# Optimization experiments

Measured on AMD Instinct MI355X. Metric: run time of the kernel, lower is better.

## Reference

```python
import jax, jax.numpy as jnp
import numpy as np

N, E, C, R = 10000, 160000, 128, 8
D = 4 * C  # 128x0e + 128x1o -> 128*1 + 128*3
INV_SQRT3 = float(1.0 / np.sqrt(3.0))  # CG norm for 1x1->0
INV_SQRT2 = float(1.0 / np.sqrt(2.0))  # CG norm for 1x1->1 (cross)
LIN_SCALE = float(1.0 / np.sqrt(C))    # e3nn Linear fan-in normalization


def _split(x):
    # l-blocked layout: [*, C] scalars then [*, C, 3] vectors
    return x[:, :C], x[:, C:].reshape(x.shape[0], C, 3)


def _merge(f0, f1):
    return jnp.concatenate([f0, f1.reshape(f1.shape[0], 3 * C)], axis=-1)


def _eq_linear(x, W0, W1):
    # equivariant linear: independent channel mixing per l
    f0, f1 = _split(x)
    return _merge((f0 @ W0) * LIN_SCALE, jnp.einsum('eci,cd->edi', f1, W1) * LIN_SCALE)


def _radial_weights(e, Wm1, Wm2, Wm3, Wm4):
    # radial MLP [R]->64->64->64->[5*C]; silu, no bias (e3nn FullyConnectedNet style)
    h = jax.nn.silu(e @ Wm1)
    h = jax.nn.silu(h @ Wm2)
    h = jax.nn.silu(h @ Wm3)
    return (h @ Wm4).reshape(-1, 5, C)  # 5 TP paths x C channels (uvu depthwise)


def setup_inputs() -> dict:
    key = jax.random.key(0)
    k = jax.random.split(key, 14)
    f32 = jnp.float32
    return {
        'node_features': jax.random.normal(k[0], (N, D), f32),
        'edge_features': jax.random.normal(k[1], (E, D), f32),
        'edge_attrs': jax.random.normal(k[2], (E, 4), f32),      # sh l=0 (1) + l=1 (3)
        'edge_embedding': jax.random.normal(k[3], (E, R), f32),  # radial basis
        'sender': jax.random.randint(k[4], (E,), 0, N, jnp.int32),
        'receiver': jax.random.randint(k[5], (E,), 0, N, jnp.int32),
        'Wm1': jax.random.normal(k[6], (R, 64), f32) * float(1.0 / np.sqrt(R)),
        'Wm2': jax.random.normal(k[7], (64, 64), f32) * 0.125,
        'Wm3': jax.random.normal(k[8], (64, 64), f32) * 0.125,
        'Wm4': jax.random.normal(k[9], (64, 5 * C), f32) * 0.125,
        'res_W0': jax.random.normal(k[10], (C, C), f32),
        'res_W1': jax.random.normal(k[11], (C, C), f32),
        'skip_W0': jax.random.normal(k[12], (C, C), f32),
        'skip_W1': jax.random.normal(k[13], (C, C), f32),
    }


def reference(node_features, edge_features, edge_attrs, edge_embedding,
              sender, receiver, Wm1, Wm2, Wm3, Wm4,
              res_W0, res_W1, skip_W0, skip_W1):
    # per-edge radial weights [E, 5, C]
    w = _radial_weights(edge_embedding, Wm1, Wm2, Wm3, Wm4)
    # gather + combine sender/receiver/edge features (all irreps_in)
    comb = node_features[sender] + node_features[receiver] + edge_features
    x0, x1 = _split(comb)                       # [E, C], [E, C, 3]
    sh0, sh1 = edge_attrs[:, 0], edge_attrs[:, 1:4]
    # depthwise (uvu) equivariant tensor product, 5 CG paths
    m0 = (w[:, 0] * x0 * sh0[:, None]
          + w[:, 1] * jnp.einsum('eci,ei->ec', x1, sh1) * INV_SQRT3)
    m1 = (w[:, 2, :, None] * x1 * sh0[:, None, None]
          + w[:, 3, :, None] * x0[:, :, None] * sh1[:, None, :]
          + w[:, 4, :, None] * jnp.cross(x1, sh1[:, None, :]) * INV_SQRT2)
    messages = _merge(m0, m1)                   # [E, D]
    # scatter-add aggregation (fixed num_segments for jit; original uses max+1)
    agg = jax.ops.segment_sum(messages, receiver, num_segments=N)
    out = agg + _eq_linear(agg, res_W0, res_W1)              # residual block
    out = out + _eq_linear(node_features, skip_W0, skip_W1)  # skip connection
    return out
```

## Files before the change

### kernel.cpp

```cpp
#include <hip/hip_runtime.h>

#define NN 10000
#define NE 160000

typedef unsigned short u16;
typedef __bf16 bf16x8 __attribute__((ext_vector_type(8)));
typedef float f32x4 __attribute__((ext_vector_type(4)));

#define INV_SQRT3 0.57735026918962576451f
#define INV_SQRT2 0.70710678118654752440f
#define LIN_SCALE 0.08838834764831845f

#define H3_OFF    0
#define WM4_OFF   20480000
#define WSW_OFF   20561920
#define CNT_OFF   20692992
#define ROFF_OFF  20733952
#define CUR_OFF   20774912
#define EL_OFF    20815872

__device__ __forceinline__ u16 f2bf(float f){
  union { float f; unsigned u; } v; v.f = f;
  unsigned r = v.u + 0x7fffu + ((v.u >> 16) & 1u);
  return (u16)(r >> 16);
}
__device__ __forceinline__ float silu_f(float x){
  return x / (1.f + __expf(-x));
}

union Frag { uint4 u4; bf16x8 bf; };

__global__ __launch_bounds__(256) void prep_weights(
    const float* __restrict__ Wm4, const float* __restrict__ rW0, const float* __restrict__ rW1,
    const float* __restrict__ sW0, const float* __restrict__ sW1,
    u16* __restrict__ wm4s, u16* __restrict__ wsw){
  int t  = blockIdx.x * blockDim.x + threadIdx.x;
  int nt = gridDim.x * blockDim.x;
  for (int idx = t; idx < 40960; idx += nt){
    int jj = idx & 7; int lane = (idx >> 3) & 63; int blk = idx >> 9;
    int ks = blk & 1; int ct = blk >> 1;
    int k = ks*32 + ((lane >> 4) << 3) + jj;
    int col = ct*16 + (lane & 15);
    wm4s[idx] = f2bf(Wm4[k*640 + col]);
  }
  const float* Ws[4] = { rW0, rW1, sW0, sW1 };
  for (int m = 0; m < 4; ++m){
    const float* src = Ws[m];
    u16* dst = wsw + m*16384;
    for (int idx = t; idx < 16384; idx += nt){
      int jj = idx & 7; int lane = (idx >> 3) & 63; int blk = idx >> 9;
      int ks = blk & 3; int ct = blk >> 2;
      int k = ks*32 + ((lane >> 4) << 3) + jj;
      int col = ct*16 + (lane & 15);
      dst[idx] = f2bf(src[k*128 + col]);
    }
  }
}

__global__ __launch_bounds__(256) void csr_zero(int* __restrict__ cnt){
  int t = blockIdx.x * blockDim.x + threadIdx.x;
  if (t < 10240) cnt[t] = 0;
}

__global__ __launch_bounds__(256) void csr_count(const int* __restrict__ rcv, int* __restrict__ cnt){
  int e = blockIdx.x * blockDim.x + threadIdx.x;
  if (e < NE) atomicAdd(&cnt[rcv[e]], 1);
}

__global__ __launch_bounds__(256) void csr_scan(const int* __restrict__ cnt,
                                                int* __restrict__ roff, int* __restrict__ cur){
  __shared__ int s_part[256];
  int t = threadIdx.x;
  int base = t * 40;
  int local = 0;
  for (int i = 0; i < 40; ++i){
    int idx = base + i;
    local += (idx < NN) ? cnt[idx] : 0;
  }
  s_part[t] = local;
  __syncthreads();
  for (int d = 1; d < 256; d <<= 1){
    int v = (t >= d) ? s_part[t - d] : 0;
    __syncthreads();
    s_part[t] += v;
    __syncthreads();
  }
  int run = (t == 0) ? 0 : s_part[t - 1];
  for (int i = 0; i < 40; ++i){
    int idx = base + i;
    if (idx < NN){
      roff[idx] = run;
      cur[idx]  = run;
      run += cnt[idx];
    }
  }
  if (t == 0) roff[NN] = NE;
}

__global__ __launch_bounds__(256) void csr_scatter(const int* __restrict__ rcv,
                                                   int* __restrict__ cur, int* __restrict__ elist){
  int e = blockIdx.x * blockDim.x + threadIdx.x;
  if (e < NE){
    int r = rcv[e];
    int p = atomicAdd(&cur[r], 1);
    elist[p] = e;
  }
}

__global__ __launch_bounds__(256) void zero_agg(float* __restrict__ agg){
  int t = blockIdx.x * blockDim.x + threadIdx.x;
  f32x4* p = (f32x4*)agg;
  const int n4 = NN*512/4;
  for (int i = t; i < n4; i += gridDim.x * blockDim.x){
    f32x4 z = {0.f,0.f,0.f,0.f}; p[i] = z;
  }
}

__global__ __launch_bounds__(256) void radial_h3_kernel(
    const float* __restrict__ emb, const float* __restrict__ Wm1,
    const float* __restrict__ Wm2, const float* __restrict__ Wm3,
    u16* __restrict__ h3){
  __shared__ float s_emb[64*12];
  __shared__ float s_w1[8*64];
  __shared__ float s_w2[64*68];
  __shared__ float s_w3[64*68];
  __shared__ float s_ha[64*65];
  __shared__ float s_hb[64*65];
  int t = threadIdx.x;
  int e0 = blockIdx.x * 64;
  if (t < 64){
    const float4* src = (const float4*)(emb + (size_t)(e0 + t)*8);
    float4 v0 = src[0], v1 = src[1];
    float* r = s_emb + t*12;
    r[0]=v0.x; r[1]=v0.y; r[2]=v0.z; r[3]=v0.w;
    r[4]=v1.x; r[5]=v1.y; r[6]=v1.z; r[7]=v1.w;
  }
  for (int idx = t; idx < 512; idx += 256) s_w1[idx] = Wm1[idx];
  for (int idx = t; idx < 4096; idx += 256){
    int k = idx >> 6, d = idx & 63;
    s_w2[k*68 + d] = Wm2[idx];
    s_w3[k*68 + d] = Wm3[idx];
  }
  __syncthreads();
  int p  = t >> 3;
  int dg = t & 7;
  int ea = 2*p, eb = 2*p + 1;
  float acc0[8], acc1[8];
  #pragma unroll
  for (int j = 0; j < 8; ++j){ acc0[j]=0.f; acc1[j]=0.f; }
  #pragma unroll
  for (int k = 0; k < 8; ++k){
    float h0 = s_emb[ea*12 + k], h1 = s_emb[eb*12 + k];
    #pragma unroll
    for (int j = 0; j < 8; ++j){
      float wv = s_w1[k*64 + dg*8 + j];
      acc0[j] = fmaf(h0, wv, acc0[j]); acc1[j] = fmaf(h1, wv, acc1[j]);
    }
  }
  #pragma unroll
  for (int j = 0; j < 8; ++j){
    s_ha[ea*65 + dg*8 + j] = silu_f(acc0[j]);
    s_ha[eb*65 + dg*8 + j] = silu_f(acc1[j]);
  }
  __syncthreads();
  #pragma unroll
  for (int j = 0; j < 8; ++j){ acc0[j]=0.f; acc1[j]=0.f; }
  #pragma unroll 4
  for (int k = 0; k < 64; ++k){
    float h0 = s_ha[ea*65 + k], h1 = s_ha[eb*65 + k];
    float wv[8];
    *(f32x4*)&wv[0] = *(const f32x4*)&s_w2[k*68 + dg*8];
    *(f32x4*)&wv[4] = *(const f32x4*)&s_w2[k*68 + dg*8 + 4];
    #pragma unroll
    for (int j = 0; j < 8; ++j){
      acc0[j] = fmaf(h0, wv[j], acc0[j]); acc1[j] = fmaf(h1, wv[j], acc1[j]);
    }
  }
  #pragma unroll
  for (int j = 0; j < 8; ++j){
    s_hb[ea*65 + dg*8 + j] = silu_f(acc0[j]);
    s_hb[eb*65 + dg*8 + j] = silu_f(acc1[j]);
  }
  __syncthreads();
  #pragma unroll
  for (int j = 0; j < 8; ++j){ acc0[j]=0.f; acc1[j]=0.f; }
  #pragma unroll 4
  for (int k = 0; k < 64; ++k){
    float h0 = s_hb[ea*65 + k], h1 = s_hb[eb*65 + k];
    float wv[8];
    *(f32x4*)&wv[0] = *(const f32x4*)&s_w3[k*68 + dg*8];
    *(f32x4*)&wv[4] = *(const f32x4*)&s_w3[k*68 + dg*8 + 4];
    #pragma unroll
    for (int j = 0; j < 8; ++j){
      acc0[j] = fmaf(h0, wv[j], acc0[j]); acc1[j] = fmaf(h1, wv[j], acc1[j]);
    }
  }
  union { u16 s[8]; uint4 v; } o0, o1;
  #pragma unroll
  for (int j = 0; j < 8; ++j){
    o0.s[j] = f2bf(silu_f(acc0[j]));
    o1.s[j] = f2bf(silu_f(acc1[j]));
  }
  *(uint4*)(h3 + (size_t)(e0 + ea)*64 + dg*8) = o0.v;
  *(uint4*)(h3 + (size_t)(e0 + eb)*64 + dg*8) = o1.v;
}

__global__ __launch_bounds__(256) void edge_msg_kernel(
    const float* __restrict__ nf, const float* __restrict__ ef, const float* __restrict__ attrs,
    const int* __restrict__ snd, const int* __restrict__ rcv,
    const u16* __restrict__ h3, const u16* __restrict__ wm4s,
    const int* __restrict__ elist, float* __restrict__ agg){
  __shared__ float s_w[16*650];
  __shared__ int s_eid[16];
  __shared__ int s_rcv[16];
  int t = threadIdx.x;
  int lane = t & 63, wave = t >> 6;
  int e0 = blockIdx.x << 4;
  if (t < 16){
    int eg = elist[e0 + t];
    s_eid[t] = eg;
    s_rcv[t] = rcv[eg];
  }
  __syncthreads();
  Frag a0f, a1f;
  const u16* h3r = h3 + (size_t)s_eid[lane & 15]*64 + ((lane >> 4) << 3);
  a0f.u4 = *(const uint4*)(h3r);
  a1f.u4 = *(const uint4*)(h3r + 32);
  int colb = lane & 15;
  int rowb = (lane >> 4) << 2;
  #pragma unroll
  for (int i = 0; i < 10; ++i){
    int ct = wave*10 + i;
    const u16* bp = wm4s + ((size_t)ct*128 + lane)*8;
    Frag b0f, b1f;
    b0f.u4 = *(const uint4*)(bp);
    b1f.u4 = *(const uint4*)(bp + 512);
    f32x4 acc = {0.f,0.f,0.f,0.f};
    acc = __builtin_amdgcn_mfma_f32_16x16x32_bf16(a0f.bf, b0f.bf, acc, 0, 0, 0);
    acc = __builtin_amdgcn_mfma_f32_16x16x32_bf16(a1f.bf, b1f.bf, acc, 0, 0, 0);
    int cb = ct*16 + colb;
    #pragma unroll
    for (int r = 0; r < 4; ++r) s_w[(rowb + r)*650 + cb] = acc[r];
  }
  __syncthreads();
  int er = t >> 4, l16 = t & 15;
  int eg = s_eid[er];
  int si = snd[eg], ri = s_rcv[er];
  float4 at = *(const float4*)(attrs + (size_t)eg*4);
  float sh0 = at.x, s1x = at.y, s1y = at.z, s1z = at.w;
  const float* ps = nf + (size_t)si*512;
  const float* pr = nf + (size_t)ri*512;
  const float* pe = ef + (size_t)eg*512;
  const float* wr = s_w + er*650;
  float m0[8], m1x[8], m1y[8], m1z[8];
  #pragma unroll
  for (int j = 0; j < 8; ++j){
    int c = j*16 + l16;
    float x0 = ps[c] + pr[c] + pe[c];
    int vb = 128 + 3*c;
    float xa = ps[vb]   + pr[vb]   + pe[vb];
    float xv = ps[vb+1] + pr[vb+1] + pe[vb+1];
    float xc = ps[vb+2] + pr[vb+2] + pe[vb+2];
    float w0 = wr[c], w1 = wr[128 + c], w2 = wr[256 + c], w3 = wr[384 + c], w4 = wr[512 + c];
    float dot = xa*s1x + xv*s1y + xc*s1z;
    m0[j] = w0*x0*sh0 + w1*dot*INV_SQRT3;
    float cr0 = xv*s1z - xc*s1y;
    float cr1 = xc*s1x - xa*s1z;
    float cr2 = xa*s1y - xv*s1x;
    m1x[j] = w2*xa*sh0 + w3*x0*s1x + w4*cr0*INV_SQRT2;
    m1y[j] = w2*xv*sh0 + w3*x0*s1y + w4*cr1*INV_SQRT2;
    m1z[j] = w2*xc*sh0 + w3*x0*s1z + w4*cr2*INV_SQRT2;
  }
  __syncthreads();
  float* mr = s_w + er*520;
  #pragma unroll
  for (int j = 0; j < 8; ++j){
    int c = j*16 + l16;
    int vb = 128 + 3*c;
    mr[c]      = m0[j];
    mr[vb]     = m1x[j];
    mr[vb + 1] = m1y[j];
    mr[vb + 2] = m1z[j];
  }
  __syncthreads();
  float sum0 = 0.f, sum1 = 0.f;
  #pragma unroll
  for (int r = 0; r < 16; ++r){
    sum0 += s_w[r*520 + t];
    sum1 += s_w[r*520 + t + 256];
    if (r == 15 || s_rcv[r] != s_rcv[r + 1]){
      float* ar = agg + (size_t)s_rcv[r]*512;
      unsafeAtomicAdd(ar + t,       sum0);
      unsafeAtomicAdd(ar + t + 256, sum1);
      sum0 = 0.f; sum1 = 0.f;
    }
  }
}

__global__ __launch_bounds__(256) void out_kernel(
    const float* __restrict__ nf, const u16* __restrict__ wsw, float* __restrict__ out){
  __shared__ u16 s_a0[16*136];
  __shared__ u16 s_a1[3][16*136];
  __shared__ u16 s_n0[16*136];
  __shared__ u16 s_n1[3][16*136];
  int t = threadIdx.x;
  int lane = t & 63, wave = t >> 6;
  int n0b = blockIdx.x << 4;
  int nr = t >> 4, l16 = t & 15;
  int node = n0b + nr;
  const float* arow = out + (size_t)node*512;
  const float* nrow = nf  + (size_t)node*512;
  #pragma unroll
  for (int jj = 0; jj < 8; ++jj){
    int c = l16 + jj*16;
    s_a0[nr*136 + c] = f2bf(arow[c]);
    s_n0[nr*136 + c] = f2bf(nrow[c]);
    #pragma unroll
    for (int i = 0; i < 3; ++i){
      s_a1[i][nr*136 + c] = f2bf(arow[128 + 3*c + i]);
      s_n1[i][nr*136 + c] = f2bf(nrow[128 + 3*c + i]);
    }
  }
  __syncthreads();
  int m15 = lane & 15, quad = lane >> 4;
  int aoff = m15*136 + (quad << 3);
  #pragma unroll
  for (int i8 = 0; i8 < 8; ++i8){
    int tt = wave*8 + i8;
    const u16 *Ag, *An, *Bg, *Bn;
    int dt, vi = 0;
    bool scalar = (tt < 8);
    if (scalar){ dt = tt; Ag = s_a0; An = s_n0; Bg = wsw; Bn = wsw + 2*16384; }
    else { vi = (tt - 8) >> 3; dt = (tt - 8) & 7; Ag = s_a1[vi]; An = s_n1[vi]; Bg = wsw + 16384; Bn = wsw + 3*16384; }
    f32x4 acc = {0.f,0.f,0.f,0.f};
    #pragma unroll
    for (int ks = 0; ks < 4; ++ks){
      Frag a, b;
      a.u4 = *(const uint4*)(Ag + aoff + ks*32);
      b.u4 = *(const uint4*)(Bg + ((size_t)(dt*4 + ks)*64 + lane)*8);
      acc = __builtin_amdgcn_mfma_f32_16x16x32_bf16(a.bf, b.bf, acc, 0, 0, 0);
    }
    #pragma unroll
    for (int ks = 0; ks < 4; ++ks){
      Frag a, b;
      a.u4 = *(const uint4*)(An + aoff + ks*32);
      b.u4 = *(const uint4*)(Bn + ((size_t)(dt*4 + ks)*64 + lane)*8);
      acc = __builtin_amdgcn_mfma_f32_16x16x32_bf16(a.bf, b.bf, acc, 0, 0, 0);
    }
    int d = dt*16 + m15;
    int idx = scalar ? d : (128 + 3*d + vi);
    #pragma unroll
    for (int r = 0; r < 4; ++r){
      int nd = n0b + quad*4 + r;
      float val = acc[r]*LIN_SCALE + out[(size_t)nd*512 + idx];
      out[(size_t)nd*512 + idx] = val;
    }
  }
}

extern "C" void kernel_launch(void* const* d_in, const int* in_sizes, int n_in,
                              void* d_out, int out_size, void* d_ws, size_t ws_size,
                              hipStream_t stream){
  (void)in_sizes; (void)n_in; (void)out_size; (void)ws_size;
  const float* nf    = (const float*)d_in[0];
  const float* ef    = (const float*)d_in[1];
  const float* attrs = (const float*)d_in[2];
  const float* emb   = (const float*)d_in[3];
  const int* snd     = (const int*)d_in[4];
  const int* rcv     = (const int*)d_in[5];
  const float* Wm1   = (const float*)d_in[6];
  const float* Wm2   = (const float*)d_in[7];
  const float* Wm3   = (const float*)d_in[8];
  const float* Wm4   = (const float*)d_in[9];
  const float* rW0   = (const float*)d_in[10];
  const float* rW1   = (const float*)d_in[11];
  const float* sW0   = (const float*)d_in[12];
  const float* sW1   = (const float*)d_in[13];
  char* ws  = (char*)d_ws;
  u16* h3    = (u16*)(ws + H3_OFF);
  u16* wm4s  = (u16*)(ws + WM4_OFF);
  u16* wsw   = (u16*)(ws + WSW_OFF);
  int* cnt   = (int*)(ws + CNT_OFF);
  int* roff  = (int*)(ws + ROFF_OFF);
  int* cur   = (int*)(ws + CUR_OFF);
  int* elist = (int*)(ws + EL_OFF);
  float* out = (float*)d_out;

  prep_weights<<<dim3(80), dim3(256), 0, stream>>>(Wm4, rW0, rW1, sW0, sW1, wm4s, wsw);
  csr_zero<<<dim3(40), dim3(256), 0, stream>>>(cnt);
  csr_count<<<dim3((NE + 255)/256), dim3(256), 0, stream>>>(rcv, cnt);
  csr_scan<<<dim3(1), dim3(256), 0, stream>>>(cnt, roff, cur);
  csr_scatter<<<dim3((NE + 255)/256), dim3(256), 0, stream>>>(rcv, cur, elist);
  zero_agg<<<dim3(1280), dim3(256), 0, stream>>>(out);
  radial_h3_kernel<<<dim3(NE/64), dim3(256), 0, stream>>>(emb, Wm1, Wm2, Wm3, h3);
  edge_msg_kernel<<<dim3(NE/16), dim3(256), 0, stream>>>(nf, ef, attrs, snd, rcv, h3, wm4s, elist, out);
  out_kernel<<<dim3(NN/16), dim3(256), 0, stream>>>(nf, wsw, out);
}
```

Measured before the change: 680.0 us.

## Run radial MLP on bf16 MFMA in CSR order with fragment-packed output

Replaces the scalar-FMA radial MLP with bf16 MFMA matmuls, one wave per 16 edges. It gathers embeddings in the receiver-sorted edge order and writes h3 already in MFMA A-fragment layout, so the edge message kernel reads it contiguously instead of gathering by edge id. The csr_zero launch is folded into prep_weights, which also pre-swizzles Wm1-3 into bf16. The costs are lower precision in the first layers (embeddings and hidden activations now bf16) and added prep work.

```diff
diff --git a/kernel.cpp b/kernel.cpp
--- a/kernel.cpp
+++ b/kernel.cpp
@@ -18,6 +18,9 @@
 #define ROFF_OFF  20733952
 #define CUR_OFF   20774912
 #define EL_OFF    20815872
+#define W1F_OFF   21455872
+#define W2F_OFF   21459968
+#define W3F_OFF   21468160
 
 __device__ __forceinline__ u16 f2bf(float f){
   union { float f; unsigned u; } v; v.f = f;
@@ -33,15 +36,33 @@
 __global__ __launch_bounds__(256) void prep_weights(
     const float* __restrict__ Wm4, const float* __restrict__ rW0, const float* __restrict__ rW1,
     const float* __restrict__ sW0, const float* __restrict__ sW1,
-    u16* __restrict__ wm4s, u16* __restrict__ wsw){
+    const float* __restrict__ Wm1, const float* __restrict__ Wm2, const float* __restrict__ Wm3,
+    u16* __restrict__ wm4s, u16* __restrict__ wsw,
+    u16* __restrict__ w1f, u16* __restrict__ w2f, u16* __restrict__ w3f,
+    int* __restrict__ cnt){
   int t  = blockIdx.x * blockDim.x + threadIdx.x;
   int nt = gridDim.x * blockDim.x;
+  if (t < 10240) cnt[t] = 0;
   for (int idx = t; idx < 40960; idx += nt){
     int jj = idx & 7; int lane = (idx >> 3) & 63; int blk = idx >> 9;
     int ks = blk & 1; int ct = blk >> 1;
     int k = ks*32 + ((lane >> 4) << 3) + jj;
     int col = ct*16 + (lane & 15);
     wm4s[idx] = f2bf(Wm4[k*640 + col]);
+  }
+  for (int idx = t; idx < 2048; idx += nt){
+    int jj = idx & 7; int lane = (idx >> 3) & 63; int ct = idx >> 9;
+    int k = ((lane >> 4) << 3) + jj;
+    int col = ct*16 + (lane & 15);
+    w1f[idx] = (k < 8) ? f2bf(Wm1[k*64 + col]) : (u16)0;
+  }
+  for (int idx = t; idx < 4096; idx += nt){
+    int jj = idx & 7; int lane = (idx >> 3) & 63; int blk = idx >> 9;
+    int ks = blk & 1; int ct = blk >> 1;
+    int k = ks*32 + ((lane >> 4) << 3) + jj;
+    int col = ct*16 + (lane & 15);
+    w2f[idx] = f2bf(Wm2[k*64 + col]);
+    w3f[idx] = f2bf(Wm3[k*64 + col]);
   }
   const float* Ws[4] = { rW0, rW1, sW0, sW1 };
   for (int m = 0; m < 4; ++m){
@@ -57,11 +78,6 @@
   }
 }
 
-__global__ __launch_bounds__(256) void csr_zero(int* __restrict__ cnt){
-  int t = blockIdx.x * blockDim.x + threadIdx.x;
-  if (t < 10240) cnt[t] = 0;
-}
-
 __global__ __launch_bounds__(256) void csr_count(const int* __restrict__ rcv, int* __restrict__ cnt){
   int e = blockIdx.x * blockDim.x + threadIdx.x;
   if (e < NE) atomicAdd(&cnt[rcv[e]], 1);
@@ -116,99 +132,101 @@
   }
 }
 
-__global__ __launch_bounds__(256) void radial_h3_kernel(
-    const float* __restrict__ emb, const float* __restrict__ Wm1,
-    const float* __restrict__ Wm2, const float* __restrict__ Wm3,
-    u16* __restrict__ h3){
-  __shared__ float s_emb[64*12];
-  __shared__ float s_w1[8*64];
-  __shared__ float s_w2[64*68];
-  __shared__ float s_w3[64*68];
-  __shared__ float s_ha[64*65];
-  __shared__ float s_hb[64*65];
+__global__ __launch_bounds__(256) void radial_mfma_kernel(
+    const float* __restrict__ emb, const int* __restrict__ elist,
+    const u16* __restrict__ w1f, const u16* __restrict__ w2f, const u16* __restrict__ w3f,
+    u16* __restrict__ h3f){
+  __shared__ u16 s_w1[2048];
+  __shared__ u16 s_w2[4096];
+  __shared__ u16 s_w3[4096];
+  __shared__ u16 s_h[4][16*72];
   int t = threadIdx.x;
-  int e0 = blockIdx.x * 64;
-  if (t < 64){
-    const float4* src = (const float4*)(emb + (size_t)(e0 + t)*8);
-    float4 v0 = src[0], v1 = src[1];
-    float* r = s_emb + t*12;
-    r[0]=v0.x; r[1]=v0.y; r[2]=v0.z; r[3]=v0.w;
-    r[4]=v1.x; r[5]=v1.y; r[6]=v1.z; r[7]=v1.w;
-  }
-  for (int idx = t; idx < 512; idx += 256) s_w1[idx] = Wm1[idx];
-  for (int idx = t; idx < 4096; idx += 256){
-    int k = idx >> 6, d = idx & 63;
-    s_w2[k*68 + d] = Wm2[idx];
-    s_w3[k*68 + d] = Wm3[idx];
-  }
-  __syncthreads();
-  int p  = t >> 3;
-  int dg = t & 7;
-  int ea = 2*p, eb = 2*p + 1;
-  float acc0[8], acc1[8];
-  #pragma unroll
-  for (int j = 0; j < 8; ++j){ acc0[j]=0.f; acc1[j]=0.f; }
-  #pragma unroll
-  for (int k = 0; k < 8; ++k){
-    float h0 = s_emb[ea*12 + k], h1 = s_emb[eb*12 + k];
-    #pragma unroll
-    for (int j = 0; j < 8; ++j){
-      float wv = s_w1[k*64 + dg*8 + j];
-      acc0[j] = fmaf(h0, wv, acc0[j]); acc1[j] = fmaf(h1, wv, acc1[j]);
-    }
-  }
-  #pragma unroll
-  for (int j = 0; j < 8; ++j){
-    s_ha[ea*65 + dg*8 + j] = silu_f(acc0[j]);
-    s_ha[eb*65 + dg*8 + j] = silu_f(acc1[j]);
-  }
-  __syncthreads();
-  #pragma unroll
-  for (int j = 0; j < 8; ++j){ acc0[j]=0.f; acc1[j]=0.f; }
-  #pragma unroll 4
-  for (int k = 0; k < 64; ++k){
-    float h0 = s_ha[ea*65 + k], h1 = s_ha[eb*65 + k];
-    float wv[8];
-    *(f32x4*)&wv[0] = *(const f32x4*)&s_w2[k*68 + dg*8];
-    *(f32x4*)&wv[4] = *(const f32x4*)&s_w2[k*68 + dg*8 + 4];
-    #pragma unroll
-    for (int j = 0; j < 8; ++j){
-      acc0[j] = fmaf(h0, wv[j], acc0[j]); acc1[j] = fmaf(h1, wv[j], acc1[j]);
-    }
-  }
-  #pragma unroll
-  for (int j = 0; j < 8; ++j){
-    s_hb[ea*65 + dg*8 + j] = silu_f(acc0[j]);
-    s_hb[eb*65 + dg*8 + j] = silu_f(acc1[j]);
-  }
-  __syncthreads();
-  #pragma unroll
-  for (int j = 0; j < 8; ++j){ acc0[j]=0.f; acc1[j]=0.f; }
-  #pragma unroll 4
-  for (int k = 0; k < 64; ++k){
-    float h0 = s_hb[ea*65 + k], h1 = s_hb[eb*65 + k];
-    float wv[8];
-    *(f32x4*)&wv[0] = *(const f32x4*)&s_w3[k*68 + dg*8];
-    *(f32x4*)&wv[4] = *(const f32x4*)&s_w3[k*68 + dg*8 + 4];
-    #pragma unroll
-    for (int j = 0; j < 8; ++j){
-      acc0[j] = fmaf(h0, wv[j], acc0[j]); acc1[j] = fmaf(h1, wv[j], acc1[j]);
-    }
-  }
-  union { u16 s[8]; uint4 v; } o0, o1;
-  #pragma unroll
-  for (int j = 0; j < 8; ++j){
-    o0.s[j] = f2bf(silu_f(acc0[j]));
-    o1.s[j] = f2bf(silu_f(acc1[j]));
-  }
-  *(uint4*)(h3 + (size_t)(e0 + ea)*64 + dg*8) = o0.v;
-  *(uint4*)(h3 + (size_t)(e0 + eb)*64 + dg*8) = o1.v;
+  int lane = t & 63, wave = t >> 6;
+  for (int i = t; i < 256; i += 256) ((uint4*)s_w1)[i] = ((const uint4*)w1f)[i];
+  for (int i = t; i < 512; i += 256) ((uint4*)s_w2)[i] = ((const uint4*)w2f)[i];
+  for (int i = t; i < 512; i += 256) ((uint4*)s_w3)[i] = ((const uint4*)w3f)[i];
+  __syncthreads();
+  int tid = blockIdx.x*4 + wave;
+  int l15 = lane & 15, q = lane >> 4;
+  u16* sh = s_h[wave];
+  Frag a;
+  a.u4.x = 0; a.u4.y = 0; a.u4.z = 0; a.u4.w = 0;
+  if (q == 0){
+    int eid = elist[tid*16 + l15];
+    const float* er = emb + (size_t)eid*8;
+    float4 v0 = *(const float4*)er;
+    float4 v1 = *(const float4*)(er + 4);
+    union { u16 s[8]; uint4 v; } pk;
+    pk.s[0]=f2bf(v0.x); pk.s[1]=f2bf(v0.y); pk.s[2]=f2bf(v0.z); pk.s[3]=f2bf(v0.w);
+    pk.s[4]=f2bf(v1.x); pk.s[5]=f2bf(v1.y); pk.s[6]=f2bf(v1.z); pk.s[7]=f2bf(v1.w);
+    a.u4 = pk.v;
+  }
+  #pragma unroll
+  for (int ct = 0; ct < 4; ++ct){
+    Frag b; b.u4 = ((const uint4*)s_w1)[ct*64 + lane];
+    f32x4 acc = {0.f,0.f,0.f,0.f};
+    acc = __builtin_amdgcn_mfma_f32_16x16x32_bf16(a.bf, b.bf, acc, 0, 0, 0);
+    #pragma unroll
+    for (int r = 0; r < 4; ++r)
+      sh[(q*4 + r)*72 + ct*16 + l15] = f2bf(silu_f(acc[r]));
+  }
+  asm volatile("s_waitcnt lgkmcnt(0)" ::: "memory");
+  __builtin_amdgcn_sched_barrier(0);
+  Frag a0, a1;
+  a0.u4 = *(const uint4*)(sh + l15*72 + q*8);
+  a1.u4 = *(const uint4*)(sh + l15*72 + q*8 + 32);
+  float h2[4][4];
+  #pragma unroll
+  for (int ct = 0; ct < 4; ++ct){
+    Frag b0, b1;
+    b0.u4 = ((const uint4*)s_w2)[(ct*2 + 0)*64 + lane];
+    b1.u4 = ((const uint4*)s_w2)[(ct*2 + 1)*64 + lane];
+    f32x4 acc = {0.f,0.f,0.f,0.f};
+    acc = __builtin_amdgcn_mfma_f32_16x16x32_bf16(a0.bf, b0.bf, acc, 0, 0, 0);
+    acc = __builtin_amdgcn_mfma_f32_16x16x32_bf16(a1.bf, b1.bf, acc, 0, 0, 0);
+    #pragma unroll
+    for (int r = 0; r < 4; ++r) h2[ct][r] = silu_f(acc[r]);
+  }
+  #pragma unroll
+  for (int ct = 0; ct < 4; ++ct)
+    #pragma unroll
+    for (int r = 0; r < 4; ++r)
+      sh[(q*4 + r)*72 + ct*16 + l15] = f2bf(h2[ct][r]);
+  asm volatile("s_waitcnt lgkmcnt(0)" ::: "memory");
+  __builtin_amdgcn_sched_barrier(0);
+  a0.u4 = *(const uint4*)(sh + l15*72 + q*8);
+  a1.u4 = *(const uint4*)(sh + l15*72 + q*8 + 32);
+  float h3v[4][4];
+  #pragma unroll
+  for (int ct = 0; ct < 4; ++ct){
+    Frag b0, b1;
+    b0.u4 = ((const uint4*)s_w3)[(ct*2 + 0)*64 + lane];
+    b1.u4 = ((const uint4*)s_w3)[(ct*2 + 1)*64 + lane];
+    f32x4 acc = {0.f,0.f,0.f,0.f};
+    acc = __builtin_amdgcn_mfma_f32_16x16x32_bf16(a0.bf, b0.bf, acc, 0, 0, 0);
+    acc = __builtin_amdgcn_mfma_f32_16x16x32_bf16(a1.bf, b1.bf, acc, 0, 0, 0);
+    #pragma unroll
+    for (int r = 0; r < 4; ++r) h3v[ct][r] = silu_f(acc[r]);
+  }
+  #pragma unroll
+  for (int ct = 0; ct < 4; ++ct)
+    #pragma unroll
+    for (int r = 0; r < 4; ++r)
+      sh[(q*4 + r)*72 + ct*16 + l15] = f2bf(h3v[ct][r]);
+  asm volatile("s_waitcnt lgkmcnt(0)" ::: "memory");
+  __builtin_amdgcn_sched_barrier(0);
+  Frag o0, o1;
+  o0.u4 = *(const uint4*)(sh + l15*72 + q*8);
+  o1.u4 = *(const uint4*)(sh + l15*72 + q*8 + 32);
+  uint4* dst = (uint4*)(h3f + (size_t)tid*1024 + lane*16);
+  dst[0] = o0.u4;
+  dst[1] = o1.u4;
 }
 
 __global__ __launch_bounds__(256) void edge_msg_kernel(
     const float* __restrict__ nf, const float* __restrict__ ef, const float* __restrict__ attrs,
     const int* __restrict__ snd, const int* __restrict__ rcv,
-    const u16* __restrict__ h3, const u16* __restrict__ wm4s,
+    const u16* __restrict__ h3f, const u16* __restrict__ wm4s,
     const int* __restrict__ elist, float* __restrict__ agg){
   __shared__ float s_w[16*650];
   __shared__ int s_eid[16];
@@ -221,11 +239,10 @@
     s_eid[t] = eg;
     s_rcv[t] = rcv[eg];
   }
-  __syncthreads();
   Frag a0f, a1f;
-  const u16* h3r = h3 + (size_t)s_eid[lane & 15]*64 + ((lane >> 4) << 3);
-  a0f.u4 = *(const uint4*)(h3r);
-  a1f.u4 = *(const uint4*)(h3r + 32);
+  const u16* hp = h3f + (size_t)blockIdx.x*1024 + (size_t)lane*16;
+  a0f.u4 = *(const uint4*)(hp);
+  a1f.u4 = *(const uint4*)(hp + 8);
   int colb = lane & 15;
   int rowb = (lane >> 4) << 2;
   #pragma unroll
@@ -377,22 +394,25 @@
   const float* sW0   = (const float*)d_in[12];
   const float* sW1   = (const float*)d_in[13];
   char* ws  = (char*)d_ws;
-  u16* h3    = (u16*)(ws + H3_OFF);
+  u16* h3f   = (u16*)(ws + H3_OFF);
   u16* wm4s  = (u16*)(ws + WM4_OFF);
   u16* wsw   = (u16*)(ws + WSW_OFF);
   int* cnt   = (int*)(ws + CNT_OFF);
   int* roff  = (int*)(ws + ROFF_OFF);
   int* cur   = (int*)(ws + CUR_OFF);
   int* elist = (int*)(ws + EL_OFF);
+  u16* w1f   = (u16*)(ws + W1F_OFF);
+  u16* w2f   = (u16*)(ws + W2F_OFF);
+  u16* w3f   = (u16*)(ws + W3F_OFF);
   float* out = (float*)d_out;
 
-  prep_weights<<<dim3(80), dim3(256), 0, stream>>>(Wm4, rW0, rW1, sW0, sW1, wm4s, wsw);
-  csr_zero<<<dim3(40), dim3(256), 0, stream>>>(cnt);
+  prep_weights<<<dim3(80), dim3(256), 0, stream>>>(Wm4, rW0, rW1, sW0, sW1, Wm1, Wm2, Wm3,
+                                                   wm4s, wsw, w1f, w2f, w3f, cnt);
   csr_count<<<dim3((NE + 255)/256), dim3(256), 0, stream>>>(rcv, cnt);
   csr_scan<<<dim3(1), dim3(256), 0, stream>>>(cnt, roff, cur);
   csr_scatter<<<dim3((NE + 255)/256), dim3(256), 0, stream>>>(rcv, cur, elist);
   zero_agg<<<dim3(1280), dim3(256), 0, stream>>>(out);
-  radial_h3_kernel<<<dim3(NE/64), dim3(256), 0, stream>>>(emb, Wm1, Wm2, Wm3, h3);
-  edge_msg_kernel<<<dim3(NE/16), dim3(256), 0, stream>>>(nf, ef, attrs, snd, rcv, h3, wm4s, elist, out);
+  radial_mfma_kernel<<<dim3(NE/64), dim3(256), 0, stream>>>(emb, elist, w1f, w2f, w3f, h3f);
+  edge_msg_kernel<<<dim3(NE/16), dim3(256), 0, stream>>>(nf, ef, attrs, snd, rcv, h3f, wm4s, elist, out);
   out_kernel<<<dim3(NN/16), dim3(256), 0, stream>>>(nf, wsw, out);
 }
```

After: 634.4 us. 6.7% less time.
